# Kernel tuning notes

Measured on AMD Instinct MI355X. Metric: run time of the kernel, lower is better.

## Reference

```python
import jax, jax.numpy as jnp
import numpy as np

COMMITMENT_COST = 1.0


def setup_inputs() -> dict:
    key = jax.random.key(0)
    k1, k2 = jax.random.split(key)
    B, D, H, W = 32, 256, 32, 32
    K = 1024
    z = jax.random.normal(k1, (B, D, H, W), dtype=jnp.float32)
    # torch init: uniform(-1/K, 1/K)
    codebook = jax.random.uniform(k2, (K, D), dtype=jnp.float32,
                                  minval=-1.0 / K, maxval=1.0 / K)
    return {"z": z, "codebook": codebook}


def reference(z, codebook):
    B, D, H, W = z.shape
    # (B, D, H, W) -> (B, H, W, D) -> (N, D)
    zp = jnp.transpose(z, (0, 2, 3, 1))
    zf = zp.reshape(-1, D)
    # squared euclidean distances (N, K): ||z||^2 + ||e||^2 - 2 z.e
    d = (jnp.sum(zf * zf, axis=1, keepdims=True)
         + jnp.sum(codebook * codebook, axis=1)
         - 2.0 * jnp.matmul(zf, codebook.T))
    idx = jnp.argmin(d, axis=1)                    # (N,)
    zq = codebook[idx].reshape(B, H, W, D)         # gather
    vq_loss = jnp.mean((jax.lax.stop_gradient(zq) - zp) ** 2)
    commitment_loss = jnp.mean((zq - jax.lax.stop_gradient(zp)) ** 2)
    loss = vq_loss + COMMITMENT_COST * commitment_loss
    # straight-through estimator
    zq_st = zp + jax.lax.stop_gradient(zq - zp)
    zq_out = jnp.transpose(zq_st, (0, 3, 1, 2))    # back to (B, D, H, W)
    indices = idx.reshape(B, H, W)
    return zq_out, indices, loss
```

## Files before the change

kernel.cpp:

```cpp
#include <hip/hip_runtime.h>

#define NPOS 32768
#define DDIM 256
#define KCODE 1024
#define HW 1024
#define BSTRIDE (256*1024)
#define OUT0_SIZE 8388608
#define OUT1_SIZE 32768

#define WS_ET     0
#define WS_ZN2    262144
#define WS_EN     327680
#define WS_PACKED 328704

__global__ void vq_prep(const float* __restrict__ z,
                        const float* __restrict__ cb,
                        float* __restrict__ ws_f,
                        unsigned long long* __restrict__ packed,
                        float* __restrict__ loss_slot) {
    __shared__ float tile[64][65];
    int bx = blockIdx.x;
    int t  = threadIdx.x;

    if (bx < 256) {
        int p = t >> 1, h = t & 1;
        int n = bx * 128 + p;
        int b = n >> 10, hw = n & 1023;
        const float* base = z + (size_t)b * BSTRIDE + hw + (size_t)(h * 128) * HW;
        float r[8];
        #pragma unroll
        for (int j = 0; j < 8; ++j) {
            float v = base[(size_t)j * HW];
            r[j] = __fmul_rn(v, v);
        }
        #pragma unroll
        for (int i = 8; i < 128; i += 8) {
            #pragma unroll
            for (int j = 0; j < 8; ++j) {
                float v = base[(size_t)(i + j) * HW];
                r[j] = __fadd_rn(r[j], __fmul_rn(v, v));
            }
        }
        float half_s = __fadd_rn(
            __fadd_rn(__fadd_rn(r[0], r[1]), __fadd_rn(r[2], r[3])),
            __fadd_rn(__fadd_rn(r[4], r[5]), __fadd_rn(r[6], r[7])));
        ws_f[WS_ZN2 + 2 * n + h] = half_s;
        if (h == 0) packed[n] = 0xFFFFFFFFFFFFFFFFull;
        if (bx == 0 && t == 0) *loss_slot = 0.0f;
    } else if (bx < 260) {
        int k = (bx - 256) * 256 + t;
        const float* row = cb + (size_t)k * DDIM;
        float half_s[2];
        #pragma unroll
        for (int h = 0; h < 2; ++h) {
            const float* p2 = row + h * 128;
            float r[8];
            #pragma unroll
            for (int j = 0; j < 8; ++j) r[j] = __fmul_rn(p2[j], p2[j]);
            #pragma unroll
            for (int i = 8; i < 128; i += 8) {
                #pragma unroll
                for (int j = 0; j < 8; ++j)
                    r[j] = __fadd_rn(r[j], __fmul_rn(p2[i + j], p2[i + j]));
            }
            half_s[h] = __fadd_rn(
                __fadd_rn(__fadd_rn(r[0], r[1]), __fadd_rn(r[2], r[3])),
                __fadd_rn(__fadd_rn(r[4], r[5]), __fadd_rn(r[6], r[7])));
        }
        ws_f[WS_EN + k] = __fadd_rn(half_s[0], half_s[1]);
    } else {
        int bt = bx - 260;
        int k0 = (bt & 15) * 64;
        int d0 = (bt >> 4) * 64;
        float* et = ws_f + WS_ET;
        #pragma unroll
        for (int p = 0; p < 4; ++p) {
            int r  = p * 16 + (t >> 4);
            int c4 = (t & 15) * 4;
            float4 v = *reinterpret_cast<const float4*>(
                cb + (size_t)(k0 + r) * DDIM + d0 + c4);
            tile[r][c4] = v.x; tile[r][c4+1] = v.y;
            tile[r][c4+2] = v.z; tile[r][c4+3] = v.w;
        }
        __syncthreads();
        #pragma unroll
        for (int s = 0; s < 16; ++s) {
            int dd = s * 4 + (t >> 6);
            int kk = t & 63;
            et[(size_t)(d0 + dd) * KCODE + k0 + kk] = tile[kk][dd];
        }
    }
}

#define BM 128
#define BN 256
#define BK 16
#define BSKEW(k) ((k) + ((k) >> 3))

__launch_bounds__(512, 4)
__global__ void vq_argmin(const float* __restrict__ z,
                          const float* __restrict__ ws_f,
                          unsigned long long* __restrict__ packed) {
    __shared__ float As[BK][128];
    __shared__ float Bs[BK][288];

    const float* ET  = ws_f + WS_ET;
    const float* zn2 = ws_f + WS_ZN2;
    const float* enW = ws_f + WS_EN;

    int t  = threadIdx.x;
    int tx = t & 31;
    int ty = t >> 5;
    int bc = blockIdx.x & 3;
    int bm = blockIdx.x >> 2;
    int kc = bc * BN;
    int n0 = bm * BM;
    int b  = n0 >> 10, hw0 = n0 & 1023;
    const float* zb = z + (size_t)b * BSTRIDE + hw0;

    float acc[8][8];
    #pragma unroll
    for (int j = 0; j < 8; ++j)
        #pragma unroll
        for (int c = 0; c < 8; ++c) acc[j][c] = 0.0f;

    for (int d0 = 0; d0 < DDIM; d0 += BK) {
        __syncthreads();
        {
            int dk = t >> 5, p4 = (t & 31) << 2;
            float4 v = *reinterpret_cast<const float4*>(
                zb + (size_t)(d0 + dk) * HW + p4);
            As[dk][p4] = v.x; As[dk][p4+1] = v.y;
            As[dk][p4+2] = v.z; As[dk][p4+3] = v.w;
        }
        #pragma unroll
        for (int i = 0; i < 2; ++i) {
            int q = t + i * 512;
            int dk = q >> 6, m = q & 63;
            float4 v = *reinterpret_cast<const float4*>(
                ET + (size_t)(d0 + dk) * KCODE + kc + 4 * m);
            int ph = BSKEW(4 * m);
            *reinterpret_cast<float4*>(&Bs[dk][ph]) = v;
        }
        __syncthreads();

        #pragma unroll
        for (int dk = 0; dk < BK; ++dk) {
            float4 a0 = *reinterpret_cast<const float4*>(&As[dk][ty * 8]);
            float4 a1 = *reinterpret_cast<const float4*>(&As[dk][ty * 8 + 4]);
            float4 b0 = *reinterpret_cast<const float4*>(&Bs[dk][9 * tx]);
            float4 b1 = *reinterpret_cast<const float4*>(&Bs[dk][9 * tx + 4]);
            float a[8]  = {a0.x, a0.y, a0.z, a0.w, a1.x, a1.y, a1.z, a1.w};
            float bb[8] = {b0.x, b0.y, b0.z, b0.w, b1.x, b1.y, b1.z, b1.w};
            #pragma unroll
            for (int j = 0; j < 8; ++j)
                #pragma unroll
                for (int c = 0; c < 8; ++c)
                    acc[j][c] = fmaf(a[j], bb[c], acc[j][c]);
        }
    }

    float znr[8];
    #pragma unroll
    for (int j = 0; j < 8; ++j) {
        int n = n0 + ty * 8 + j;
        znr[j] = __fadd_rn(zn2[2 * n], zn2[2 * n + 1]);
    }
    float4 e0 = *reinterpret_cast<const float4*>(enW + kc + 8 * tx);
    float4 e1 = *reinterpret_cast<const float4*>(enW + kc + 8 * tx + 4);
    float en8[8] = {e0.x, e0.y, e0.z, e0.w, e1.x, e1.y, e1.z, e1.w};

    float m1[8];
    int   i1[8];
    #pragma unroll
    for (int j = 0; j < 8; ++j) { m1[j] = 1e30f; i1[j] = 0; }
    #pragma unroll
    for (int c = 0; c < 8; ++c) {
        int k = kc + 8 * tx + c;
        float ek = en8[c];
        #pragma unroll
        for (int j = 0; j < 8; ++j) {
            float t1 = __fadd_rn(znr[j], ek);
            float d  = __fsub_rn(t1, __fmul_rn(2.0f, acc[j][c]));
            if (d < m1[j]) { m1[j] = d; i1[j] = k; }
        }
    }

    #pragma unroll
    for (int j = 0; j < 8; ++j) {
        float a1v = m1[j];
        int   ii  = i1[j];
        #pragma unroll
        for (int off = 1; off < 32; off <<= 1) {
            float o1 = __shfl_xor(a1v, off, 32);
            int   oi = __shfl_xor(ii, off, 32);
            if (o1 < a1v || (o1 == a1v && oi < ii)) { a1v = o1; ii = oi; }
        }
        if (tx == 0) {
            unsigned long long key =
                ((unsigned long long)__float_as_uint(a1v) << 32) |
                (unsigned long long)(unsigned)ii;
            atomicMin(&packed[n0 + ty * 8 + j], key);
        }
    }
}

__global__ void vq_gather(const float* __restrict__ z,
                          const float* __restrict__ cb,
                          const unsigned long long* __restrict__ packed,
                          float* __restrict__ out,
                          float* __restrict__ loss) {
    int t  = threadIdx.x;
    int p  = t & 63, dc = t >> 6;
    int n  = blockIdx.x * 64 + p;
    int b  = n >> 10, hw = n & 1023;
    int k  = (int)(unsigned)(packed[n] & 0xFFFFFFFFull);
    size_t off = (size_t)b * BSTRIDE + hw + (size_t)(dc * 64) * HW;
    const float* e  = cb + (size_t)k * DDIM + dc * 64;
    const float* zp = z + off;
    float* op = out + off;
    float s = 0.0f;
    #pragma unroll 4
    for (int d4 = 0; d4 < 16; ++d4) {
        float4 ev = *reinterpret_cast<const float4*>(e + 4 * d4);
        float evs[4] = {ev.x, ev.y, ev.z, ev.w};
        #pragma unroll
        for (int q = 0; q < 4; ++q) {
            int d = 4 * d4 + q;
            float zv = zp[(size_t)d * HW];
            op[(size_t)d * HW] = evs[q];
            float df = evs[q] - zv;
            s = fmaf(df, df, s);
        }
    }
    if (dc == 0) out[OUT0_SIZE + n] = (float)k;

    #pragma unroll
    for (int o = 32; o > 0; o >>= 1) s += __shfl_down(s, o);
    __shared__ float red[4];
    int lane = t & 63, w = t >> 6;
    if (lane == 0) red[w] = s;
    __syncthreads();
    if (t == 0) {
        float tot = (red[0] + red[1] + red[2] + red[3]) * (2.0f / 8388608.0f);
        atomicAdd(loss, tot);
    }
}

extern "C" void kernel_launch(void* const* d_in, const int* in_sizes, int n_in,
                              void* d_out, int out_size, void* d_ws, size_t ws_size,
                              hipStream_t stream) {
    const float* z  = (const float*)d_in[0];
    const float* cb = (const float*)d_in[1];
    float* out  = (float*)d_out;
    float* ws_f = (float*)d_ws;
    unsigned long long* packed =
        (unsigned long long*)(ws_f + WS_PACKED);
    float* loss = out + OUT0_SIZE + OUT1_SIZE;

    vq_prep<<<324, 256, 0, stream>>>(z, cb, ws_f, packed, loss);
    vq_argmin<<<(NPOS / BM) * (KCODE / BN), 512, 0, stream>>>(z, ws_f, packed);
    vq_gather<<<NPOS / 64, 256, 0, stream>>>(z, cb, packed, out, loss);
}
```

Before: 311.5 us.

## Load z operand directly per wavefront as uniform loads, drop A shared tile

Restructures the argmin GEMM so each 64-lane wavefront owns 16 positions and every lane computes 4 codes. The z operand is no longer staged in LDS; each wave reads its 16 wave-uniform z values straight from global memory (readfirstlane makes the address uniform, which may let the compiler use scalar loads). The B tile loses its skew padding, and the min-reduction now spans a full 64-lane wave. The aim is to cut LDS traffic and per-thread LDS reads, at the cost of repeated global loads of z in the inner loop and a 64-step shuffle reduction per position.

After: 306.6 us. Within noise of the previous version (-1.6%).

```diff
diff --git a/kernel.cpp b/kernel.cpp
--- a/kernel.cpp
+++ b/kernel.cpp
@@ -95,112 +95,92 @@
 #define BM 128
 #define BN 256
 #define BK 16
-#define BSKEW(k) ((k) + ((k) >> 3))
 
 __launch_bounds__(512, 4)
 __global__ void vq_argmin(const float* __restrict__ z,
                           const float* __restrict__ ws_f,
                           unsigned long long* __restrict__ packed) {
-    __shared__ float As[BK][128];
-    __shared__ float Bs[BK][288];
+    __shared__ float Bs[BK][BN];
 
     const float* ET  = ws_f + WS_ET;
     const float* zn2 = ws_f + WS_ZN2;
     const float* enW = ws_f + WS_EN;
 
-    int t  = threadIdx.x;
-    int tx = t & 31;
-    int ty = t >> 5;
+    int t    = threadIdx.x;
+    int lane = t & 63;
+    int wq   = __builtin_amdgcn_readfirstlane(t >> 6);
     int bc = blockIdx.x & 3;
     int bm = blockIdx.x >> 2;
     int kc = bc * BN;
     int n0 = bm * BM;
     int b  = n0 >> 10, hw0 = n0 & 1023;
     const float* zb = z + (size_t)b * BSTRIDE + hw0;
-
-    float acc[8][8];
+    const float* za = zb + wq * 16;
+
+    float acc[16][4];
     #pragma unroll
-    for (int j = 0; j < 8; ++j)
-        #pragma unroll
-        for (int c = 0; c < 8; ++c) acc[j][c] = 0.0f;
+    for (int j = 0; j < 16; ++j)
+        #pragma unroll
+        for (int c = 0; c < 4; ++c) acc[j][c] = 0.0f;
 
     for (int d0 = 0; d0 < DDIM; d0 += BK) {
         __syncthreads();
-        {
-            int dk = t >> 5, p4 = (t & 31) << 2;
-            float4 v = *reinterpret_cast<const float4*>(
-                zb + (size_t)(d0 + dk) * HW + p4);
-            As[dk][p4] = v.x; As[dk][p4+1] = v.y;
-            As[dk][p4+2] = v.z; As[dk][p4+3] = v.w;
-        }
         #pragma unroll
         for (int i = 0; i < 2; ++i) {
             int q = t + i * 512;
             int dk = q >> 6, m = q & 63;
             float4 v = *reinterpret_cast<const float4*>(
                 ET + (size_t)(d0 + dk) * KCODE + kc + 4 * m);
-            int ph = BSKEW(4 * m);
-            *reinterpret_cast<float4*>(&Bs[dk][ph]) = v;
+            *reinterpret_cast<float4*>(&Bs[dk][4 * m]) = v;
         }
         __syncthreads();
 
         #pragma unroll
         for (int dk = 0; dk < BK; ++dk) {
-            float4 a0 = *reinterpret_cast<const float4*>(&As[dk][ty * 8]);
-            float4 a1 = *reinterpret_cast<const float4*>(&As[dk][ty * 8 + 4]);
-            float4 b0 = *reinterpret_cast<const float4*>(&Bs[dk][9 * tx]);
-            float4 b1 = *reinterpret_cast<const float4*>(&Bs[dk][9 * tx + 4]);
-            float a[8]  = {a0.x, a0.y, a0.z, a0.w, a1.x, a1.y, a1.z, a1.w};
-            float bb[8] = {b0.x, b0.y, b0.z, b0.w, b1.x, b1.y, b1.z, b1.w};
-            #pragma unroll
-            for (int j = 0; j < 8; ++j)
+            float4 b4 = *reinterpret_cast<const float4*>(&Bs[dk][4 * lane]);
+            const float* ar = za + (size_t)(d0 + dk) * HW;
+            float4 a0 = *reinterpret_cast<const float4*>(ar);
+            float4 a1 = *reinterpret_cast<const float4*>(ar + 4);
+            float4 a2 = *reinterpret_cast<const float4*>(ar + 8);
+            float4 a3 = *reinterpret_cast<const float4*>(ar + 12);
+            float a[16] = {a0.x, a0.y, a0.z, a0.w, a1.x, a1.y, a1.z, a1.w,
+                           a2.x, a2.y, a2.z, a2.w, a3.x, a3.y, a3.z, a3.w};
+            float bb[4] = {b4.x, b4.y, b4.z, b4.w};
+            #pragma unroll
+            for (int j = 0; j < 16; ++j)
                 #pragma unroll
-                for (int c = 0; c < 8; ++c)
+                for (int c = 0; c < 4; ++c)
                     acc[j][c] = fmaf(a[j], bb[c], acc[j][c]);
         }
     }
 
-    float znr[8];
+    float4 e4 = *reinterpret_cast<const float4*>(enW + kc + 4 * lane);
+    float en4[4] = {e4.x, e4.y, e4.z, e4.w};
+
     #pragma unroll
-    for (int j = 0; j < 8; ++j) {
-        int n = n0 + ty * 8 + j;
-        znr[j] = __fadd_rn(zn2[2 * n], zn2[2 * n + 1]);
-    }
-    float4 e0 = *reinterpret_cast<const float4*>(enW + kc + 8 * tx);
-    float4 e1 = *reinterpret_cast<const float4*>(enW + kc + 8 * tx + 4);
-    float en8[8] = {e0.x, e0.y, e0.z, e0.w, e1.x, e1.y, e1.z, e1.w};
-
-    float m1[8];
-    int   i1[8];
-    #pragma unroll
-    for (int j = 0; j < 8; ++j) { m1[j] = 1e30f; i1[j] = 0; }
-    #pragma unroll
-    for (int c = 0; c < 8; ++c) {
-        int k = kc + 8 * tx + c;
-        float ek = en8[c];
-        #pragma unroll
-        for (int j = 0; j < 8; ++j) {
-            float t1 = __fadd_rn(znr[j], ek);
+    for (int j = 0; j < 16; ++j) {
+        int n = n0 + wq * 16 + j;
+        float znr = __fadd_rn(zn2[2 * n], zn2[2 * n + 1]);
+        float m1 = 1e30f;
+        int   i1 = 0;
+        #pragma unroll
+        for (int c = 0; c < 4; ++c) {
+            int k = kc + 4 * lane + c;
+            float t1 = __fadd_rn(znr, en4[c]);
             float d  = __fsub_rn(t1, __fmul_rn(2.0f, acc[j][c]));
-            if (d < m1[j]) { m1[j] = d; i1[j] = k; }
-        }
-    }
-
-    #pragma unroll
-    for (int j = 0; j < 8; ++j) {
-        float a1v = m1[j];
-        int   ii  = i1[j];
-        #pragma unroll
-        for (int off = 1; off < 32; off <<= 1) {
-            float o1 = __shfl_xor(a1v, off, 32);
-            int   oi = __shfl_xor(ii, off, 32);
-            if (o1 < a1v || (o1 == a1v && oi < ii)) { a1v = o1; ii = oi; }
-        }
-        if (tx == 0) {
+            if (d < m1) { m1 = d; i1 = k; }
+        }
+        #pragma unroll
+        for (int off = 1; off < 64; off <<= 1) {
+            float o1 = __shfl_xor(m1, off, 64);
+            int   oi = __shfl_xor(i1, off, 64);
+            if (o1 < m1 || (o1 == m1 && oi < i1)) { m1 = o1; i1 = oi; }
+        }
+        if (lane == 0) {
             unsigned long long key =
-                ((unsigned long long)__float_as_uint(a1v) << 32) |
-                (unsigned long long)(unsigned)ii;
-            atomicMin(&packed[n0 + ty * 8 + j], key);
+                ((unsigned long long)__float_as_uint(m1) << 32) |
+                (unsigned long long)(unsigned)i1;
+            atomicMin(&packed[n], key);
         }
     }
 }
```
